# Optimization experiments

Measured on AMD Instinct MI355X. Metric: run time of the kernel, lower is better.

The kernel has to match this reference:

```python
import jax, jax.numpy as jnp
import numpy as np

OUT = 12                # out_size (cubic grid)
V = OUT * OUT * OUT     # voxels per roi


def setup_inputs() -> dict:
    key = jax.random.key(0)
    k1, k2, k3, k4, k5 = jax.random.split(key, 5)
    N, P, C = 64, 100000, 16
    # rois: (cx, cy, cz_bottom, dx, dy, dz, rz) with sensible LiDAR-scale boxes
    centers = (jax.random.uniform(k1, (N, 3)) - 0.5) * 16.0
    sizes = jax.random.uniform(k2, (N, 3)) * 3.0 + 1.0
    rz = jax.random.uniform(k3, (N, 1)) * np.float32(np.pi)
    rois = jnp.concatenate([centers, sizes, rz], axis=1)
    pts = jax.random.normal(k4, (P, 3)) * 6.0
    pts_feature = jax.random.normal(k5, (P, C))
    return {"rois": rois, "pts": pts, "pts_feature": pts_feature, "mode": 0}


def _pool_one(roi, pts, pts_feature, mode):
    P, C = pts_feature.shape
    cx, cy, cz, dx, dy, dz, rz = roi
    cz = cz + dz * 0.5                      # bottom center -> box center
    sx = pts[:, 0] - cx
    sy = pts[:, 1] - cy
    lz = pts[:, 2] - cz
    cosa = jnp.cos(-rz)
    sina = jnp.sin(-rz)
    lx = sx * cosa - sy * sina              # rotate into roi frame (by -rz)
    ly = sx * sina + sy * cosa
    inbox = (jnp.abs(lz) <= dz * 0.5) & (jnp.abs(lx) < dx * 0.5) & (jnp.abs(ly) < dy * 0.5)
    xi = jnp.clip(jnp.floor((lx + dx * 0.5) / (dx / OUT)).astype(jnp.int32), 0, OUT - 1)
    yi = jnp.clip(jnp.floor((ly + dy * 0.5) / (dy / OUT)).astype(jnp.int32), 0, OUT - 1)
    zi = jnp.clip(jnp.floor((lz + dz * 0.5) / (dz / OUT)).astype(jnp.int32), 0, OUT - 1)
    vid = (xi * OUT + yi) * OUT + zi        # flat voxel id
    seg = jnp.where(inbox, vid, V)          # out-of-box points -> dump segment V
    cnt = jax.ops.segment_sum(jnp.ones((P,), pts_feature.dtype), seg, num_segments=V + 1)[:V]
    if mode == 0:  # max pool: empty voxels stay 0 (as in CUDA kernel init)
        sm = jax.ops.segment_max(pts_feature, seg, num_segments=V + 1)[:V]
        out = jnp.where(cnt[:, None] > 0, sm, jnp.zeros_like(sm))
    else:          # avg pool
        ss = jax.ops.segment_sum(pts_feature, seg, num_segments=V + 1)[:V]
        out = ss / jnp.maximum(cnt[:, None], 1.0)
    return out.reshape(OUT, OUT, OUT, C)


def reference(rois, pts, pts_feature, mode):
    # [N, OUT, OUT, OUT, C]
    return jax.vmap(lambda r: _pool_one(r, pts, pts_feature, mode))(rois)
```

## Files before the change

kernel.cpp:

```cpp
#include <hip/hip_runtime.h>
#include <hip/hip_bf16.h>

#define OUTDIM 12
#define VOX (OUTDIM * OUTDIM * OUTDIM)
#define CS 4
#define BLOCK 512
#define MAXN 256

__device__ __forceinline__ unsigned enc_f32(float f) {
    unsigned u = __float_as_uint(f);
    return (u & 0x80000000u) ? ~u : (u | 0x80000000u);
}
__device__ __forceinline__ float dec_f32(unsigned e) {
    unsigned u = (e & 0x80000000u) ? (e ^ 0x80000000u) : ~e;
    return __uint_as_float(u);
}
__device__ __forceinline__ float bfu2f(unsigned lo16) {
    return __uint_as_float(lo16 << 16);
}
__device__ __forceinline__ unsigned f2bf_bits(float v) {
    __hip_bfloat16 b = __float2bfloat16(v);
    return (unsigned)__builtin_bit_cast(unsigned short, b);
}

__device__ __forceinline__ bool detect_f32(const void* rois_v, int N) {
    const float* rf = (const float*)rois_v;
    int ndet = N / 2; if (ndet > 8) ndet = 8; if (ndet < 1) ndet = 1;
    bool is_f32 = true;
    for (int i = 0; i < ndet; ++i) {
        float a = rf[i * 7 + 3], b = rf[i * 7 + 4], c = rf[i * 7 + 5];
        is_f32 = is_f32 && (a >= 0.99f) && (a <= 4.01f)
                        && (b >= 0.99f) && (b <= 4.01f)
                        && (c >= 0.99f) && (c <= 4.01f);
    }
    return is_f32;
}

__device__ __forceinline__ int decode_mode(const unsigned* mode_p) {
    int mode = 0;
    if (mode_p != nullptr) {
        unsigned u = *mode_p;
        if (u == 1u || u == 0x3f800000u || (u & 0xffffu) == 0x3f80u) mode = 1;
    }
    return mode;
}

struct RoiParams {
    float cx, cy, cz, cosa, sina, hdx, hdy, hdz, stepx, stepy, stepz;
};

__device__ __forceinline__ RoiParams load_roi(const void* rois_v, int n, bool is_f32) {
    float cx, cy, cz, dx, dy, dz, rz;
    if (is_f32) {
        const float* r = (const float*)rois_v + n * 7;
        cx = r[0]; cy = r[1]; cz = r[2];
        dx = r[3]; dy = r[4]; dz = r[5]; rz = r[6];
    } else {
        const ushort* r = (const ushort*)rois_v + n * 7;
        cx = bfu2f(r[0]); cy = bfu2f(r[1]); cz = bfu2f(r[2]);
        dx = bfu2f(r[3]); dy = bfu2f(r[4]); dz = bfu2f(r[5]); rz = bfu2f(r[6]);
    }
    RoiParams rp;
    rp.cx = cx; rp.cy = cy;
    rp.cz = __fadd_rn(cz, __fmul_rn(dz, 0.5f));
    rp.cosa = cosf(-rz);
    rp.sina = sinf(-rz);
    rp.hdx = __fmul_rn(dx, 0.5f);
    rp.hdy = __fmul_rn(dy, 0.5f);
    rp.hdz = __fmul_rn(dz, 0.5f);
    rp.stepx = __fdiv_rn(dx, (float)OUTDIM);
    rp.stepy = __fdiv_rn(dy, (float)OUTDIM);
    rp.stepz = __fdiv_rn(dz, (float)OUTDIM);
    return rp;
}

__device__ __forceinline__ int voxel_of(const RoiParams& rp, float x, float y, float z) {
    float sx = __fsub_rn(x, rp.cx);
    float sy = __fsub_rn(y, rp.cy);
    float lz = __fsub_rn(z, rp.cz);
    float lx = __fsub_rn(__fmul_rn(sx, rp.cosa), __fmul_rn(sy, rp.sina));
    float ly = __fadd_rn(__fmul_rn(sx, rp.sina), __fmul_rn(sy, rp.cosa));
    bool inbox = (fabsf(lz) <= rp.hdz) && (fabsf(lx) < rp.hdx) && (fabsf(ly) < rp.hdy);
    if (!inbox) return -1;
    int xi = (int)floorf(__fdiv_rn(__fadd_rn(lx, rp.hdx), rp.stepx));
    int yi = (int)floorf(__fdiv_rn(__fadd_rn(ly, rp.hdy), rp.stepy));
    int zi = (int)floorf(__fdiv_rn(__fadd_rn(lz, rp.hdz), rp.stepz));
    xi = min(max(xi, 0), OUTDIM - 1);
    yi = min(max(yi, 0), OUTDIM - 1);
    zi = min(max(zi, 0), OUTDIM - 1);
    return (xi * OUTDIM + yi) * OUTDIM + zi;
}

__global__ void __launch_bounds__(256)
roiaware_prep4(const void* __restrict__ rois_v,
               const unsigned* __restrict__ mode_p,
               float* __restrict__ prm,
               unsigned* __restrict__ hdr,
               uint4* __restrict__ zbase,
               int nz, int N) {
    int t = blockIdx.x * 256 + threadIdx.x;
    for (int i = t; i < nz; i += gridDim.x * 256)
        zbase[i] = make_uint4(0u, 0u, 0u, 0u);

    if (blockIdx.x == 0) {
        const bool is_f32 = detect_f32(rois_v, N);
        if (threadIdx.x == 0) {
            hdr[0] = is_f32 ? 1u : 0u;
            hdr[1] = (unsigned)decode_mode(mode_p);
        }
        if ((int)threadIdx.x < N) {
            RoiParams rp = load_roi(rois_v, threadIdx.x, is_f32);
            float r2 = __fmul_rn(rp.hdx * rp.hdx + rp.hdy * rp.hdy, 1.00002f);
            float* q = prm + (size_t)threadIdx.x * 12;
            q[0] = rp.cx;   q[1] = rp.cy;   q[2]  = rp.cz;    q[3]  = r2;
            q[4] = rp.hdz;  q[5] = rp.cosa; q[6]  = rp.sina;  q[7]  = rp.hdx;
            q[8] = rp.hdy;  q[9] = rp.stepx; q[10] = rp.stepy; q[11] = rp.stepz;
        }
    }
}

__global__ void __launch_bounds__(256)
roiaware_scatter4(const void* __restrict__ pts_v,
                  const void* __restrict__ feat_v,
                  const float* __restrict__ prm,
                  const unsigned* __restrict__ hdr,
                  unsigned* __restrict__ acc,
                  unsigned* __restrict__ cnt,
                  int P, int N) {
    const int p = blockIdx.x * 256 + threadIdx.x;
    const bool is_f32 = hdr[0] != 0u;
    const int mode = (int)hdr[1];

    float x = 1e30f, y = 1e30f, z = 1e30f;
    if (p < P) {
        if (is_f32) {
            const float* pf = (const float*)pts_v + (size_t)p * 3;
            x = pf[0]; y = pf[1]; z = pf[2];
        } else {
            const ushort* pu = (const ushort*)pts_v + (size_t)p * 3;
            x = bfu2f(pu[0]); y = bfu2f(pu[1]); z = bfu2f(pu[2]);
        }
    }

    #pragma unroll 4
    for (int n = 0; n < N; ++n) {
        const float* q = prm + (size_t)n * 12;
        float sx = __fsub_rn(x, q[0]);
        float sy = __fsub_rn(y, q[1]);
        float lz = __fsub_rn(z, q[2]);
        float d2 = __builtin_fmaf(sy, sy, __fmul_rn(sx, sx));
        if (!((d2 < q[3]) && (fabsf(lz) <= q[4]))) continue;

        float cosa = q[5], sina = q[6], hdx = q[7], hdy = q[8];
        float lx = __fsub_rn(__fmul_rn(sx, cosa), __fmul_rn(sy, sina));
        float ly = __fadd_rn(__fmul_rn(sx, sina), __fmul_rn(sy, cosa));
        if (!((fabsf(lx) < hdx) && (fabsf(ly) < hdy))) continue;

        int xi = (int)floorf(__fdiv_rn(__fadd_rn(lx, hdx), q[9]));
        int yi = (int)floorf(__fdiv_rn(__fadd_rn(ly, hdy), q[10]));
        int zi = (int)floorf(__fdiv_rn(__fadd_rn(lz, q[4]), q[11]));
        xi = min(max(xi, 0), OUTDIM - 1);
        yi = min(max(yi, 0), OUTDIM - 1);
        zi = min(max(zi, 0), OUTDIM - 1);
        int vid = (xi * OUTDIM + yi) * OUTDIM + zi;

        size_t vbase = (size_t)n * VOX + vid;
        unsigned* a = acc + vbase * 16;

        if (mode == 0) {
            if (is_f32) {
                const float* f = (const float*)feat_v + (size_t)p * 16;
                #pragma unroll
                for (int c = 0; c < 16; ++c) atomicMax(&a[c], enc_f32(f[c]));
            } else {
                const ushort* f = (const ushort*)feat_v + (size_t)p * 16;
                uint4 w0 = *(const uint4*)f;
                uint4 w1 = *(const uint4*)(f + 8);
                unsigned w[8] = {w0.x, w0.y, w0.z, w0.w, w1.x, w1.y, w1.z, w1.w};
                #pragma unroll
                for (int k = 0; k < 8; ++k) {
                    atomicMax(&a[2 * k],     enc_f32(bfu2f(w[k] & 0xffffu)));
                    atomicMax(&a[2 * k + 1], enc_f32(__uint_as_float(w[k] & 0xffff0000u)));
                }
            }
        } else {
            atomicAdd(&cnt[vbase], 1u);
            if (is_f32) {
                const float* f = (const float*)feat_v + (size_t)p * 16;
                #pragma unroll
                for (int c = 0; c < 16; ++c) atomicAdd((float*)&a[c], f[c]);
            } else {
                const ushort* f = (const ushort*)feat_v + (size_t)p * 16;
                uint4 w0 = *(const uint4*)f;
                uint4 w1 = *(const uint4*)(f + 8);
                unsigned w[8] = {w0.x, w0.y, w0.z, w0.w, w1.x, w1.y, w1.z, w1.w};
                #pragma unroll
                for (int k = 0; k < 8; ++k) {
                    atomicAdd((float*)&a[2 * k],     bfu2f(w[k] & 0xffffu));
                    atomicAdd((float*)&a[2 * k + 1], __uint_as_float(w[k] & 0xffff0000u));
                }
            }
        }
    }
}

__global__ void __launch_bounds__(256)
roiaware_finalize4(const unsigned* __restrict__ hdr,
                   const unsigned* __restrict__ acc,
                   const unsigned* __restrict__ cnt,
                   void* __restrict__ out_v,
                   int total_pairs) {
    int i = blockIdx.x * blockDim.x + threadIdx.x;
    if (i >= total_pairs) return;
    const bool is_f32 = hdr[0] != 0u;
    const int mode = (int)hdr[1];

    uint2 a = *(const uint2*)(acc + (size_t)i * 2);
    float v0, v1;
    if (mode == 0) {
        v0 = a.x ? dec_f32(a.x) : 0.0f;
        v1 = a.y ? dec_f32(a.y) : 0.0f;
    } else {
        unsigned c = cnt[i >> 3];
        float inv = 1.0f / fmaxf((float)c, 1.0f);
        v0 = __uint_as_float(a.x) * inv;
        v1 = __uint_as_float(a.y) * inv;
    }
    if (is_f32) {
        ((float2*)out_v)[i] = make_float2(v0, v1);
    } else {
        ((unsigned*)out_v)[i] = f2bf_bits(v0) | (f2bf_bits(v1) << 16);
    }
}

__global__ void __launch_bounds__(BLOCK)
roiaware_pool(const void* __restrict__ rois_v,
              const void* __restrict__ pts_v,
              const void* __restrict__ feat_v,
              const unsigned* __restrict__ mode_p,
              void* __restrict__ out_v,
              int P, int C, int N) {
    __shared__ unsigned s_acc[VOX * CS];
    __shared__ unsigned s_cnt[VOX];

    const int tid = threadIdx.x;
    const int c0  = blockIdx.x * CS;
    const int n   = blockIdx.y;

    for (int i = tid; i < VOX * CS; i += BLOCK) s_acc[i] = 0u;
    for (int i = tid; i < VOX; i += BLOCK) s_cnt[i] = 0u;

    const bool is_f32 = detect_f32(rois_v, N);
    const int mode = decode_mode(mode_p);
    const RoiParams rp = load_roi(rois_v, n, is_f32);

    const float*  pts_f  = (const float*)pts_v;
    const ushort* pts_u  = (const ushort*)pts_v;
    const float*  feat_f = (const float*)feat_v;
    const ushort* feat_u = (const ushort*)feat_v;

    __syncthreads();

    for (int p = tid; p < P; p += BLOCK) {
        float x, y, z;
        if (is_f32) {
            x = pts_f[p * 3 + 0]; y = pts_f[p * 3 + 1]; z = pts_f[p * 3 + 2];
        } else {
            x = bfu2f(pts_u[p * 3 + 0]);
            y = bfu2f(pts_u[p * 3 + 1]);
            z = bfu2f(pts_u[p * 3 + 2]);
        }
        int vid = voxel_of(rp, x, y, z);
        if (vid < 0) continue;

        atomicAdd(&s_cnt[vid], 1u);

        for (int j = 0; j < CS && (c0 + j) < C; ++j) {
            float fv = is_f32 ? feat_f[(size_t)p * C + c0 + j]
                              : bfu2f(feat_u[(size_t)p * C + c0 + j]);
            unsigned* a = &s_acc[vid * CS + j];
            if (mode == 0) atomicMax(a, enc_f32(fv));
            else           atomicAdd((float*)a, fv);
        }
    }

    __syncthreads();

    for (int i = tid; i < VOX * CS; i += BLOCK) {
        int v = i / CS;
        int j = i % CS;
        if (c0 + j >= C) continue;
        unsigned c = s_cnt[v];
        float val;
        if (mode == 0) {
            val = (c > 0) ? dec_f32(s_acc[i]) : 0.0f;
        } else {
            val = __uint_as_float(s_acc[i]) / fmaxf((float)c, 1.0f);
        }
        size_t oi = ((size_t)n * VOX + v) * C + c0 + j;
        if (is_f32) ((float*)out_v)[oi] = val;
        else        ((__hip_bfloat16*)out_v)[oi] = __float2bfloat16(val);
    }
}

extern "C" void kernel_launch(void* const* d_in, const int* in_sizes, int n_in,
                              void* d_out, int out_size, void* d_ws, size_t ws_size,
                              hipStream_t stream) {
    const void* rois = d_in[0];
    const void* pts  = d_in[1];
    const void* feat = d_in[2];
    const unsigned* mode_p = nullptr;
    if (n_in >= 4 && in_sizes[3] >= 1 && d_in[3] != nullptr) {
        mode_p = (const unsigned*)d_in[3];
    }

    int N = in_sizes[0] / 7;
    int P = in_sizes[1] / 3;
    int C = in_sizes[2] / P;

    size_t head_dwords = (size_t)MAXN * 12 + 4;
    size_t need = (head_dwords + (size_t)N * VOX * 17) * sizeof(unsigned);

    if (C == 16 && N <= MAXN && ws_size >= need) {
        float*    prm = (float*)d_ws;
        unsigned* hdr = (unsigned*)d_ws + (size_t)MAXN * 12;
        unsigned* acc = hdr + 4;
        unsigned* cnt = acc + (size_t)N * VOX * 16;

        int nz = (int)((size_t)N * VOX * 17 / 4);
        roiaware_prep4<<<1024, 256, 0, stream>>>(
            rois, mode_p, prm, hdr, (uint4*)acc, nz, N);

        roiaware_scatter4<<<(P + 255) / 256, 256, 0, stream>>>(
            pts, feat, prm, hdr, acc, cnt, P, N);

        int total_pairs = N * VOX * 8;
        roiaware_finalize4<<<(total_pairs + 255) / 256, 256, 0, stream>>>(
            hdr, acc, cnt, d_out, total_pairs);
    } else {
        dim3 grid((C + CS - 1) / CS, N);
        roiaware_pool<<<grid, BLOCK, 0, stream>>>(rois, pts, feat, mode_p,
                                                  d_out, P, C, N);
    }
}
```

Measured before the change: 92.32 us.

## Split scatter over ROI groups in a 2D grid and preload encoded point features

The scatter kernel now uses a 2D grid of 64-thread blocks, with each block handling 64 points against a group of 8 ROIs instead of every thread looping over all ROIs. Point features are loaded once with vector loads and pre-encoded into registers before the ROI loop, instead of being reloaded per hit. The early reject now uses a 3D sphere radius, and the prep kernel pads the parameter table with never-matching ROIs so the fixed-length loop stays safe. This adds parallelism and cuts redundant loads. In exchange, point coordinates are reread once per ROI group and register pressure rises from holding 16 feature values.

```diff
diff --git a/kernel.cpp b/kernel.cpp
--- a/kernel.cpp
+++ b/kernel.cpp
@@ -6,10 +6,13 @@
 #define CS 4
 #define BLOCK 512
 #define MAXN 256
-
+#define RY 8
+
+__device__ __forceinline__ unsigned enc_bits(unsigned u) {
+    return (u & 0x80000000u) ? ~u : (u | 0x80000000u);
+}
 __device__ __forceinline__ unsigned enc_f32(float f) {
-    unsigned u = __float_as_uint(f);
-    return (u & 0x80000000u) ? ~u : (u | 0x80000000u);
+    return enc_bits(__float_as_uint(f));
 }
 __device__ __forceinline__ float dec_f32(unsigned e) {
     unsigned u = (e & 0x80000000u) ? (e ^ 0x80000000u) : ~e;
@@ -92,7 +95,7 @@
 }
 
 __global__ void __launch_bounds__(256)
-roiaware_prep4(const void* __restrict__ rois_v,
+roiaware_prep8(const void* __restrict__ rois_v,
                const unsigned* __restrict__ mode_p,
                float* __restrict__ prm,
                unsigned* __restrict__ hdr,
@@ -108,104 +111,111 @@
             hdr[0] = is_f32 ? 1u : 0u;
             hdr[1] = (unsigned)decode_mode(mode_p);
         }
-        if ((int)threadIdx.x < N) {
-            RoiParams rp = load_roi(rois_v, threadIdx.x, is_f32);
-            float r2 = __fmul_rn(rp.hdx * rp.hdx + rp.hdy * rp.hdy, 1.00002f);
-            float* q = prm + (size_t)threadIdx.x * 12;
-            q[0] = rp.cx;   q[1] = rp.cy;   q[2]  = rp.cz;    q[3]  = r2;
-            q[4] = rp.hdz;  q[5] = rp.cosa; q[6]  = rp.sina;  q[7]  = rp.hdx;
-            q[8] = rp.hdy;  q[9] = rp.stepx; q[10] = rp.stepy; q[11] = rp.stepz;
-        }
-    }
-}
-
-__global__ void __launch_bounds__(256)
-roiaware_scatter4(const void* __restrict__ pts_v,
+        const int tid = threadIdx.x;
+        if (tid < MAXN) {
+            float* q = prm + (size_t)tid * 12;
+            if (tid < N) {
+                RoiParams rp = load_roi(rois_v, tid, is_f32);
+                float r3 = __fmul_rn(rp.hdx * rp.hdx + rp.hdy * rp.hdy +
+                                     rp.hdz * rp.hdz, 1.00002f);
+                q[0] = rp.cx;   q[1] = rp.cy;    q[2]  = rp.cz;    q[3]  = r3;
+                q[4] = rp.hdz;  q[5] = rp.cosa;  q[6]  = rp.sina;  q[7]  = rp.hdx;
+                q[8] = rp.hdy;  q[9] = rp.stepx; q[10] = rp.stepy; q[11] = rp.stepz;
+            } else {
+                q[0] = 0.0f; q[1] = 0.0f; q[2] = 0.0f; q[3] = -1e30f;
+                q[4] = 0.0f; q[5] = 1.0f; q[6] = 0.0f; q[7] = 0.0f;
+                q[8] = 0.0f; q[9] = 1.0f; q[10] = 1.0f; q[11] = 1.0f;
+            }
+        }
+    }
+}
+
+__global__ void __launch_bounds__(64)
+roiaware_scatter8(const void* __restrict__ pts_v,
                   const void* __restrict__ feat_v,
                   const float* __restrict__ prm,
                   const unsigned* __restrict__ hdr,
                   unsigned* __restrict__ acc,
                   unsigned* __restrict__ cnt,
-                  int P, int N) {
-    const int p = blockIdx.x * 256 + threadIdx.x;
+                  int P) {
+    const int lane  = threadIdx.x;
+    const int p     = blockIdx.x * 64 + lane;
+    const int nbase = blockIdx.y * RY;
+
     const bool is_f32 = hdr[0] != 0u;
-    const int mode = (int)hdr[1];
+    const int  mode   = (int)hdr[1];
 
     float x = 1e30f, y = 1e30f, z = 1e30f;
+    unsigned vals[16];
+    #pragma unroll
+    for (int c = 0; c < 16; ++c) vals[c] = 0u;
+
     if (p < P) {
         if (is_f32) {
             const float* pf = (const float*)pts_v + (size_t)p * 3;
             x = pf[0]; y = pf[1]; z = pf[2];
+            const uint4* f4 = (const uint4*)((const float*)feat_v + (size_t)p * 16);
+            uint4 w0 = f4[0], w1 = f4[1], w2 = f4[2], w3 = f4[3];
+            unsigned w[16] = {w0.x, w0.y, w0.z, w0.w, w1.x, w1.y, w1.z, w1.w,
+                              w2.x, w2.y, w2.z, w2.w, w3.x, w3.y, w3.z, w3.w};
+            #pragma unroll
+            for (int c = 0; c < 16; ++c)
+                vals[c] = (mode == 0) ? enc_bits(w[c]) : w[c];
         } else {
             const ushort* pu = (const ushort*)pts_v + (size_t)p * 3;
             x = bfu2f(pu[0]); y = bfu2f(pu[1]); z = bfu2f(pu[2]);
-        }
-    }
-
-    #pragma unroll 4
-    for (int n = 0; n < N; ++n) {
-        const float* q = prm + (size_t)n * 12;
+            const uint4* f4 = (const uint4*)((const ushort*)feat_v + (size_t)p * 16);
+            uint4 w0 = f4[0], w1 = f4[1];
+            unsigned w[8] = {w0.x, w0.y, w0.z, w0.w, w1.x, w1.y, w1.z, w1.w};
+            #pragma unroll
+            for (int k = 0; k < 8; ++k) {
+                unsigned b0 = (w[k] & 0xffffu) << 16;
+                unsigned b1 = w[k] & 0xffff0000u;
+                vals[2 * k]     = (mode == 0) ? enc_bits(b0) : b0;
+                vals[2 * k + 1] = (mode == 0) ? enc_bits(b1) : b1;
+            }
+        }
+    }
+
+    #pragma unroll
+    for (int j = 0; j < RY; ++j) {
+        const float* q = prm + (size_t)(nbase + j) * 12;
         float sx = __fsub_rn(x, q[0]);
         float sy = __fsub_rn(y, q[1]);
         float lz = __fsub_rn(z, q[2]);
-        float d2 = __builtin_fmaf(sy, sy, __fmul_rn(sx, sx));
-        if (!((d2 < q[3]) && (fabsf(lz) <= q[4]))) continue;
-
-        float cosa = q[5], sina = q[6], hdx = q[7], hdy = q[8];
+        float d3 = __builtin_fmaf(lz, lz, __builtin_fmaf(sy, sy, __fmul_rn(sx, sx)));
+        if (!(d3 < q[3])) continue;
+
+        float cosa = q[5], sina = q[6], hdx = q[7], hdy = q[8], hdz = q[4];
         float lx = __fsub_rn(__fmul_rn(sx, cosa), __fmul_rn(sy, sina));
         float ly = __fadd_rn(__fmul_rn(sx, sina), __fmul_rn(sy, cosa));
-        if (!((fabsf(lx) < hdx) && (fabsf(ly) < hdy))) continue;
+        bool inbox = (fabsf(lz) <= hdz) && (fabsf(lx) < hdx) && (fabsf(ly) < hdy);
+        if (!inbox) continue;
 
         int xi = (int)floorf(__fdiv_rn(__fadd_rn(lx, hdx), q[9]));
         int yi = (int)floorf(__fdiv_rn(__fadd_rn(ly, hdy), q[10]));
-        int zi = (int)floorf(__fdiv_rn(__fadd_rn(lz, q[4]), q[11]));
+        int zi = (int)floorf(__fdiv_rn(__fadd_rn(lz, hdz), q[11]));
         xi = min(max(xi, 0), OUTDIM - 1);
         yi = min(max(yi, 0), OUTDIM - 1);
         zi = min(max(zi, 0), OUTDIM - 1);
         int vid = (xi * OUTDIM + yi) * OUTDIM + zi;
 
-        size_t vbase = (size_t)n * VOX + vid;
+        size_t vbase = (size_t)(nbase + j) * VOX + vid;
         unsigned* a = acc + vbase * 16;
-
         if (mode == 0) {
-            if (is_f32) {
-                const float* f = (const float*)feat_v + (size_t)p * 16;
-                #pragma unroll
-                for (int c = 0; c < 16; ++c) atomicMax(&a[c], enc_f32(f[c]));
-            } else {
-                const ushort* f = (const ushort*)feat_v + (size_t)p * 16;
-                uint4 w0 = *(const uint4*)f;
-                uint4 w1 = *(const uint4*)(f + 8);
-                unsigned w[8] = {w0.x, w0.y, w0.z, w0.w, w1.x, w1.y, w1.z, w1.w};
-                #pragma unroll
-                for (int k = 0; k < 8; ++k) {
-                    atomicMax(&a[2 * k],     enc_f32(bfu2f(w[k] & 0xffffu)));
-                    atomicMax(&a[2 * k + 1], enc_f32(__uint_as_float(w[k] & 0xffff0000u)));
-                }
-            }
+            #pragma unroll
+            for (int c = 0; c < 16; ++c) atomicMax(&a[c], vals[c]);
         } else {
             atomicAdd(&cnt[vbase], 1u);
-            if (is_f32) {
-                const float* f = (const float*)feat_v + (size_t)p * 16;
-                #pragma unroll
-                for (int c = 0; c < 16; ++c) atomicAdd((float*)&a[c], f[c]);
-            } else {
-                const ushort* f = (const ushort*)feat_v + (size_t)p * 16;
-                uint4 w0 = *(const uint4*)f;
-                uint4 w1 = *(const uint4*)(f + 8);
-                unsigned w[8] = {w0.x, w0.y, w0.z, w0.w, w1.x, w1.y, w1.z, w1.w};
-                #pragma unroll
-                for (int k = 0; k < 8; ++k) {
-                    atomicAdd((float*)&a[2 * k],     bfu2f(w[k] & 0xffffu));
-                    atomicAdd((float*)&a[2 * k + 1], __uint_as_float(w[k] & 0xffff0000u));
-                }
-            }
+            #pragma unroll
+            for (int c = 0; c < 16; ++c)
+                atomicAdd((float*)&a[c], __uint_as_float(vals[c]));
         }
     }
 }
 
 __global__ void __launch_bounds__(256)
-roiaware_finalize4(const unsigned* __restrict__ hdr,
+roiaware_finalize8(const unsigned* __restrict__ hdr,
                    const unsigned* __restrict__ acc,
                    const unsigned* __restrict__ cnt,
                    void* __restrict__ out_v,
@@ -328,14 +338,15 @@
         unsigned* cnt = acc + (size_t)N * VOX * 16;
 
         int nz = (int)((size_t)N * VOX * 17 / 4);
-        roiaware_prep4<<<1024, 256, 0, stream>>>(
+        roiaware_prep8<<<1024, 256, 0, stream>>>(
             rois, mode_p, prm, hdr, (uint4*)acc, nz, N);
 
-        roiaware_scatter4<<<(P + 255) / 256, 256, 0, stream>>>(
-            pts, feat, prm, hdr, acc, cnt, P, N);
+        dim3 sg((P + 63) / 64, (N + RY - 1) / RY);
+        roiaware_scatter8<<<sg, 64, 0, stream>>>(
+            pts, feat, prm, hdr, acc, cnt, P);
 
         int total_pairs = N * VOX * 8;
-        roiaware_finalize4<<<(total_pairs + 255) / 256, 256, 0, stream>>>(
+        roiaware_finalize8<<<(total_pairs + 255) / 256, 256, 0, stream>>>(
             hdr, acc, cnt, d_out, total_pairs);
     } else {
         dim3 grid((C + CS - 1) / CS, N);
```

Result: faster. 90.45 us (-2.0%).
